# Optimization experiments

Hardware: AMD Instinct MI355X
Metric: run time of the kernel (lower is better)

## Reference

```python
import jax, jax.numpy as jnp
import numpy as np

N_NODES = 100000
N_EDGES = 1200000
IN_FEATS = 64
OUT_FEATS = 64


def setup_inputs() -> dict:
    key = jax.random.key(0)
    k1, k2, k3, k4 = jax.random.split(key, 4)
    feature = jax.random.normal(k1, (N_NODES, IN_FEATS), dtype=jnp.float32)
    edge_src = jax.random.randint(k2, (N_EDGES,), 0, N_NODES, dtype=jnp.int32)
    edge_dst = jax.random.randint(k3, (N_EDGES,), 0, N_NODES, dtype=jnp.int32)
    # xavier_normal_ init for linear weight (fan_in=fan_out=64)
    std = float(np.sqrt(2.0 / (IN_FEATS + OUT_FEATS)))
    W = jax.random.normal(k4, (OUT_FEATS, IN_FEATS), dtype=jnp.float32) * std
    b = jnp.zeros((OUT_FEATS,), dtype=jnp.float32)
    return {"feature": feature, "edge_src": edge_src, "edge_dst": edge_dst, "W": W, "b": b}


def reference(feature, edge_src, edge_dst, W, b):
    # copy_src: gather source-node features per edge, then mean-reduce by dst.
    msgs = feature[edge_src]                                   # [E, d_in]
    summed = jax.ops.segment_sum(msgs, edge_dst, num_segments=N_NODES)  # [N, d_in]
    deg = jax.ops.segment_sum(jnp.ones((edge_src.shape[0],), feature.dtype),
                              edge_dst, num_segments=N_NODES)  # [N]
    h = summed / jnp.maximum(deg, 1.0)[:, None]                # mean; 0 for isolated nodes
    # apply_nodes: linear + activation
    h = jnp.einsum("nd,od->no", h, W) + b
    return jax.nn.relu(h)
```

## Files before the change

### kernel.cpp

```cpp
#include <hip/hip_runtime.h>


typedef __attribute__((ext_vector_type(8))) short short8;
typedef __attribute__((ext_vector_type(4))) float floatx4;

constexpr int kNodes = 100000;
constexpr int kEdges = 1200000;

constexpr int kBucketShift = 7;
constexpr int kBucketNodes = 1 << kBucketShift;
constexpr int kBuckets = (kNodes + kBucketNodes - 1) >> kBucketShift;

constexpr int kBinBlocks = 128;
constexpr int kEdgesPerBlock = kEdges / kBinBlocks;
constexpr int kEPT = (kEdgesPerBlock + 1023) / 1024;

constexpr int kCap = 3072;
constexpr float kFxScale = 262144.0f;
constexpr int kAccStride = 68;

constexpr int kWsFeat   = 0;
constexpr int kWsOff    = 3200000;
constexpr int kWsBinned = kWsOff + kBinBlocks * 784;

__device__ __forceinline__ unsigned bf16rne(float f) {
  unsigned u = __float_as_uint(f);
  return (u + 0x7fffu + ((u >> 16) & 1u)) >> 16;
}

__global__ __launch_bounds__(1024) void gcn_build(
    const float* __restrict__ feat,
    const int* __restrict__ src, const int* __restrict__ dst,
    int* __restrict__ ws) {
  uint2* fb16  = (uint2*)(ws + kWsFeat);
  int* offT   = ws + kWsOff;
  int* binned = ws + kWsBinned;

  __shared__ int lhist[kBuckets];
  __shared__ int sm[1024];
  __shared__ int lcur[kBuckets];

  const int tid = threadIdx.x;
  for (int i = tid; i < kBuckets; i += 1024) lhist[i] = 0;
  __syncthreads();

  const int e0 = blockIdx.x * kEdgesPerBlock;
  int es[kEPT], ed[kEPT];
  #pragma unroll
  for (int k = 0; k < kEPT; ++k) {
    const int j = tid + k * 1024;
    if (j < kEdgesPerBlock) {
      es[k] = src[e0 + j];
      ed[k] = dst[e0 + j];
      atomicAdd(&lhist[ed[k] >> kBucketShift], 1);
    }
  }

  const int t = blockIdx.x * 1024 + tid;
  for (int i = t; i < kNodes * 16; i += kBinBlocks * 1024) {
    const float* fr = feat + (size_t)(i >> 4) * 64 + (i & 15);
    uint2 p;
    p.x = bf16rne(fr[0])  | (bf16rne(fr[16]) << 16);
    p.y = bf16rne(fr[32]) | (bf16rne(fr[48]) << 16);
    fb16[i] = p;
  }
  __syncthreads();

  const int own = (tid < kBuckets) ? lhist[tid] : 0;
  sm[tid] = own;
  __syncthreads();
  for (int off = 1; off < 1024; off <<= 1) {
    int v = (tid >= off) ? sm[tid - off] : 0;
    __syncthreads();
    sm[tid] += v;
    __syncthreads();
  }
  const int excl = sm[tid] - own;
  if (tid < kBuckets) {
    lcur[tid] = excl;
    offT[blockIdx.x * 784 + tid] = excl;
  }
  if (tid == kBuckets) offT[blockIdx.x * 784 + kBuckets] = kEdgesPerBlock;
  __syncthreads();

  int* myBin = binned + blockIdx.x * kEdgesPerBlock;
  #pragma unroll
  for (int k = 0; k < kEPT; ++k) {
    const int j = tid + k * 1024;
    if (j < kEdgesPerBlock) {
      const int d = ed[k];
      const int pos = atomicAdd(&lcur[d >> kBucketShift], 1);
      myBin[pos] = es[k] | ((d & (kBucketNodes - 1)) << 17);
    }
  }
}

__global__ __launch_bounds__(1024) void gcn_aggregate(
    const int*   __restrict__ ws_in,
    const float* __restrict__ W,
    const float* __restrict__ b,
    float*       __restrict__ out) {
  const uint2* fb16  = (const uint2*)(ws_in + kWsFeat);
  const int* offT   = ws_in + kWsOff;
  const int* binned = ws_in + kWsBinned;

  __shared__ __align__(16) char uShared[kBucketNodes * 72 * 2];
  __shared__ int    accum[kBucketNodes * kAccStride];
  __shared__ int    lofs[kBucketNodes + 1];
  __shared__ int    lcur[kBucketNodes];
  __shared__ int    runL[kBinBlocks + 1];
  __shared__ int    runG[kBinBlocks];
  __shared__ int    ssm[kBinBlocks];
  __shared__ ushort Wb16[64 * 64];
  __shared__ float  bsh[64];
  int*    lsrc  = (int*)uShared;
  ushort* hsAll = (ushort*)uShared;

  const int tid = threadIdx.x;
  const int bkt = blockIdx.x;

  if (tid < kBucketNodes) lcur[tid] = 0;
  for (int i = tid; i < 4096; i += 1024) Wb16[i] = (ushort)bf16rne(W[i]);
  if (tid < 64) bsh[tid] = b[tid];
  for (int i = tid; i < kBucketNodes * kAccStride; i += 1024) accum[i] = 0;

  int len = 0;
  if (tid < kBinBlocks) {
    const int o0 = offT[tid * 784 + bkt];
    const int o1 = offT[tid * 784 + bkt + 1];
    len = o1 - o0;
    runG[tid] = tid * kEdgesPerBlock + o0;
    ssm[tid] = len;
  }
  __syncthreads();
  for (int off = 1; off < kBinBlocks; off <<= 1) {
    int v = 0;
    if (tid < kBinBlocks && tid >= off) v = ssm[tid - off];
    __syncthreads();
    if (tid < kBinBlocks) ssm[tid] += v;
    __syncthreads();
  }
  if (tid < kBinBlocks) runL[tid] = ssm[tid] - len;
  if (tid == kBinBlocks - 1) runL[kBinBlocks] = ssm[kBinBlocks - 1];
  __syncthreads();

  int sz = runL[kBinBlocks];
  if (sz > kCap) sz = kCap;

  auto mapRead = [&](int j) -> unsigned {
    int lo = 0, hi = kBinBlocks;
    #pragma unroll
    for (int it = 0; it < 7; ++it) {
      const int mid = (lo + hi) >> 1;
      if (runL[mid] <= j) lo = mid; else hi = mid;
    }
    return (unsigned)binned[runG[lo] + (j - runL[lo])];
  };

  const int j0 = tid, j1 = tid + 1024, j2 = tid + 2048;
  const bool va = j0 < sz, vb = j1 < sz, vc = j2 < sz;
  unsigned ea = 0, eb = 0, ec = 0;
  if (va) { ea = mapRead(j0); atomicAdd(&lcur[ea >> 17], 1); }
  if (vb) { eb = mapRead(j1); atomicAdd(&lcur[eb >> 17], 1); }
  if (vc) { ec = mapRead(j2); atomicAdd(&lcur[ec >> 17], 1); }
  __syncthreads();

  if (tid < 64) {
    const int a  = lcur[tid * 2];
    const int b2 = lcur[tid * 2 + 1];
    int s = a + b2;
    #pragma unroll
    for (int off = 1; off < 64; off <<= 1) {
      const int v = __shfl_up(s, off, 64);
      if (tid >= off) s += v;
    }
    const int ex1 = s - b2;
    const int ex0 = ex1 - a;
    lofs[tid * 2]     = ex0;
    lofs[tid * 2 + 1] = ex1;
    lcur[tid * 2]     = ex0;
    lcur[tid * 2 + 1] = ex1;
    if (tid == 63) lofs[kBucketNodes] = s;
  }
  __syncthreads();

  if (va) { const int p = atomicAdd(&lcur[ea >> 17], 1); lsrc[p] = (int)ea; }
  if (vb) { const int p = atomicAdd(&lcur[eb >> 17], 1); lsrc[p] = (int)eb; }
  if (vc) { const int p = atomicAdd(&lcur[ec >> 17], 1); lsrc[p] = (int)ec; }
  __syncthreads();

  const int wave = tid >> 6;
  const int lane = tid & 63;
  const int g = lane >> 4;
  const int c = lane & 15;
  {
    const int E0 = lofs[wave * 8];
    const int E1 = lofs[wave * 8 + 8];
    const int lenw = E1 - E0;
    const int jb = E0 + ((lenw * g) >> 2);
    const int je = E0 + ((lenw * (g + 1)) >> 2);
    for (int j = jb; j < je; ++j) {
      const unsigned e = (unsigned)lsrc[j];
      const int s  = (int)(e & 0x1FFFF);
      const int dL = (int)(e >> 17);
      const uint2 v = fb16[(size_t)s * 16 + c];
      int* row = accum + dL * kAccStride + c;
      atomicAdd(row + 0,  (int)(__uint_as_float(v.x << 16)          * kFxScale));
      atomicAdd(row + 16, (int)(__uint_as_float(v.x & 0xffff0000u) * kFxScale));
      atomicAdd(row + 32, (int)(__uint_as_float(v.y << 16)          * kFxScale));
      atomicAdd(row + 48, (int)(__uint_as_float(v.y & 0xffff0000u) * kFxScale));
    }
  }
  __syncthreads();

  {
    const int nd = tid >> 3;
    const int ch = tid & 7;
    const int dg = lofs[nd + 1] - lofs[nd];
    const float inv = 1.0f / (kFxScale * (float)(dg > 1 ? dg : 1));
    const int* arow = accum + nd * kAccStride + ch * 8;
    unsigned h[8];
    #pragma unroll
    for (int q = 0; q < 8; ++q) h[q] = bf16rne((float)arow[q] * inv);
    uint4 pk;
    pk.x = h[0] | (h[1] << 16);
    pk.y = h[2] | (h[3] << 16);
    pk.z = h[4] | (h[5] << 16);
    pk.w = h[6] | (h[7] << 16);
    *(uint4*)(hsAll + nd * 72 + ch * 8) = pk;
  }
  __syncthreads();

  if (tid < 512) {
    const int w8   = tid >> 6;
    const int ln   = tid & 63;
    const int quad = ln >> 4;
    const int col  = ln & 15;
    const int n0 = bkt << kBucketShift;

    const short8 a0 = *reinterpret_cast<const short8*>(
        hsAll + (w8 * 16 + col) * 72 + 0 * 32 + quad * 8);
    const short8 a1 = *reinterpret_cast<const short8*>(
        hsAll + (w8 * 16 + col) * 72 + 1 * 32 + quad * 8);

    #pragma unroll
    for (int ob = 0; ob < 4; ++ob) {
      const short8 b0 = *reinterpret_cast<const short8*>(
          Wb16 + (ob * 16 + col) * 64 + 0 * 32 + quad * 8);
      const short8 b1 = *reinterpret_cast<const short8*>(
          Wb16 + (ob * 16 + col) * 64 + 1 * 32 + quad * 8);
      floatx4 acc = {0.f, 0.f, 0.f, 0.f};
      acc = __builtin_amdgcn_mfma_f32_16x16x32_bf16(a0, b0, acc, 0, 0, 0);
      acc = __builtin_amdgcn_mfma_f32_16x16x32_bf16(a1, b1, acc, 0, 0, 0);

      const int o = ob * 16 + col;
      const float bo = bsh[o];
      #pragma unroll
      for (int r = 0; r < 4; ++r) {
        const int node = n0 + w8 * 16 + quad * 4 + r;
        if (node < kNodes) {
          const float v = acc[r] + bo;
          out[(size_t)node * 64 + o] = v > 0.0f ? v : 0.0f;
        }
      }
    }
  }
}

extern "C" void kernel_launch(void* const* d_in, const int* in_sizes, int n_in,
                              void* d_out, int out_size, void* d_ws, size_t ws_size,
                              hipStream_t stream) {
  const float* feature  = (const float*)d_in[0];
  const int*   edge_src = (const int*)  d_in[1];
  const int*   edge_dst = (const int*)  d_in[2];
  const float* W        = (const float*)d_in[3];
  const float* b        = (const float*)d_in[4];

  float* out = (float*)d_out;
  int*   ws  = (int*)d_ws;

  gcn_build<<<kBinBlocks, 1024, 0, stream>>>(feature, edge_src, edge_dst, ws);
  gcn_aggregate<<<kBuckets, 1024, 0, stream>>>(ws, W, b, out);
}
```

Before: 138.2 us.

## Accumulate per-node sums in registers instead of LDS fixed-point atomics

Assigns each 16-lane group two consecutive destination nodes within the bucket and sums their gathered bf16 source features in float registers, writing the mean directly to the bf16 staging tile. This removes the shared accumulator array, its zero-initialization, the fixed-point conversion and all per-edge LDS atomics. The trade-off is load imbalance, because work is split by node rather than evenly by edge count, and high-degree nodes serialize within a group. LDS footprint also shrinks.

```diff
diff --git a/kernel.cpp b/kernel.cpp
--- a/kernel.cpp
+++ b/kernel.cpp
@@ -16,8 +16,6 @@
 constexpr int kEPT = (kEdgesPerBlock + 1023) / 1024;
 
 constexpr int kCap = 3072;
-constexpr float kFxScale = 262144.0f;
-constexpr int kAccStride = 68;
 
 constexpr int kWsFeat   = 0;
 constexpr int kWsOff    = 3200000;
@@ -105,7 +103,6 @@
   const int* binned = ws_in + kWsBinned;
 
   __shared__ __align__(16) char uShared[kBucketNodes * 72 * 2];
-  __shared__ int    accum[kBucketNodes * kAccStride];
   __shared__ int    lofs[kBucketNodes + 1];
   __shared__ int    lcur[kBucketNodes];
   __shared__ int    runL[kBinBlocks + 1];
@@ -122,7 +119,6 @@
   if (tid < kBucketNodes) lcur[tid] = 0;
   for (int i = tid; i < 4096; i += 1024) Wb16[i] = (ushort)bf16rne(W[i]);
   if (tid < 64) bsh[tid] = b[tid];
-  for (int i = tid; i < kBucketNodes * kAccStride; i += 1024) accum[i] = 0;
 
   int len = 0;
   if (tid < kBinBlocks) {
@@ -193,41 +189,46 @@
   const int lane = tid & 63;
   const int g = lane >> 4;
   const int c = lane & 15;
+  const int nd0 = wave * 8 + g * 2;
+
+  float a00 = 0.f, a01 = 0.f, a02 = 0.f, a03 = 0.f;
+  float a10 = 0.f, a11 = 0.f, a12 = 0.f, a13 = 0.f;
+  const int sA = lofs[nd0];
+  const int sB = lofs[nd0 + 1];
+  const int sC = lofs[nd0 + 2];
+  for (int j = sA; j < sB; ++j) {
+    const unsigned e = (unsigned)lsrc[j];
+    const uint2 v = fb16[(size_t)(e & 0x1FFFF) * 16 + c];
+    a00 += __uint_as_float(v.x << 16);
+    a01 += __uint_as_float(v.x & 0xffff0000u);
+    a02 += __uint_as_float(v.y << 16);
+    a03 += __uint_as_float(v.y & 0xffff0000u);
+  }
+  for (int j = sB; j < sC; ++j) {
+    const unsigned e = (unsigned)lsrc[j];
+    const uint2 v = fb16[(size_t)(e & 0x1FFFF) * 16 + c];
+    a10 += __uint_as_float(v.x << 16);
+    a11 += __uint_as_float(v.x & 0xffff0000u);
+    a12 += __uint_as_float(v.y << 16);
+    a13 += __uint_as_float(v.y & 0xffff0000u);
+  }
+  __syncthreads();
+
   {
-    const int E0 = lofs[wave * 8];
-    const int E1 = lofs[wave * 8 + 8];
-    const int lenw = E1 - E0;
-    const int jb = E0 + ((lenw * g) >> 2);
-    const int je = E0 + ((lenw * (g + 1)) >> 2);
-    for (int j = jb; j < je; ++j) {
-      const unsigned e = (unsigned)lsrc[j];
-      const int s  = (int)(e & 0x1FFFF);
-      const int dL = (int)(e >> 17);
-      const uint2 v = fb16[(size_t)s * 16 + c];
-      int* row = accum + dL * kAccStride + c;
-      atomicAdd(row + 0,  (int)(__uint_as_float(v.x << 16)          * kFxScale));
-      atomicAdd(row + 16, (int)(__uint_as_float(v.x & 0xffff0000u) * kFxScale));
-      atomicAdd(row + 32, (int)(__uint_as_float(v.y << 16)          * kFxScale));
-      atomicAdd(row + 48, (int)(__uint_as_float(v.y & 0xffff0000u) * kFxScale));
-    }
-  }
-  __syncthreads();
-
-  {
-    const int nd = tid >> 3;
-    const int ch = tid & 7;
-    const int dg = lofs[nd + 1] - lofs[nd];
-    const float inv = 1.0f / (kFxScale * (float)(dg > 1 ? dg : 1));
-    const int* arow = accum + nd * kAccStride + ch * 8;
-    unsigned h[8];
-    #pragma unroll
-    for (int q = 0; q < 8; ++q) h[q] = bf16rne((float)arow[q] * inv);
-    uint4 pk;
-    pk.x = h[0] | (h[1] << 16);
-    pk.y = h[2] | (h[3] << 16);
-    pk.z = h[4] | (h[5] << 16);
-    pk.w = h[6] | (h[7] << 16);
-    *(uint4*)(hsAll + nd * 72 + ch * 8) = pk;
+    const int dg0 = sB - sA;
+    const int dg1 = sC - sB;
+    const float inv0 = 1.0f / (float)(dg0 > 1 ? dg0 : 1);
+    const float inv1 = 1.0f / (float)(dg1 > 1 ? dg1 : 1);
+    ushort* row0 = hsAll + nd0 * 72;
+    ushort* row1 = row0 + 72;
+    row0[c]      = (ushort)bf16rne(a00 * inv0);
+    row0[16 + c] = (ushort)bf16rne(a01 * inv0);
+    row0[32 + c] = (ushort)bf16rne(a02 * inv0);
+    row0[48 + c] = (ushort)bf16rne(a03 * inv0);
+    row1[c]      = (ushort)bf16rne(a10 * inv1);
+    row1[16 + c] = (ushort)bf16rne(a11 * inv1);
+    row1[32 + c] = (ushort)bf16rne(a12 * inv1);
+    row1[48 + c] = (ushort)bf16rne(a13 * inv1);
   }
   __syncthreads();
 
@@ -238,20 +239,20 @@
     const int col  = ln & 15;
     const int n0 = bkt << kBucketShift;
 
-    const short8 a0 = *reinterpret_cast<const short8*>(
+    const short8 af0 = *reinterpret_cast<const short8*>(
         hsAll + (w8 * 16 + col) * 72 + 0 * 32 + quad * 8);
-    const short8 a1 = *reinterpret_cast<const short8*>(
+    const short8 af1 = *reinterpret_cast<const short8*>(
         hsAll + (w8 * 16 + col) * 72 + 1 * 32 + quad * 8);
 
     #pragma unroll
     for (int ob = 0; ob < 4; ++ob) {
-      const short8 b0 = *reinterpret_cast<const short8*>(
+      const short8 bf0 = *reinterpret_cast<const short8*>(
           Wb16 + (ob * 16 + col) * 64 + 0 * 32 + quad * 8);
-      const short8 b1 = *reinterpret_cast<const short8*>(
+      const short8 bf1 = *reinterpret_cast<const short8*>(
           Wb16 + (ob * 16 + col) * 64 + 1 * 32 + quad * 8);
       floatx4 acc = {0.f, 0.f, 0.f, 0.f};
-      acc = __builtin_amdgcn_mfma_f32_16x16x32_bf16(a0, b0, acc, 0, 0, 0);
-      acc = __builtin_amdgcn_mfma_f32_16x16x32_bf16(a1, b1, acc, 0, 0, 0);
+      acc = __builtin_amdgcn_mfma_f32_16x16x32_bf16(af0, bf0, acc, 0, 0, 0);
+      acc = __builtin_amdgcn_mfma_f32_16x16x32_bf16(af1, bf1, acc, 0, 0, 0);
 
       const int o = ob * 16 + col;
       const float bo = bsh[o];
```

Measured after the change: 142.2 us. +2.9%, slower.

## Rebucket nodes into 1024 buckets of 98 and split edges evenly across slots

Applied to the files above, without the earlier changes.

Node buckets change from 128 power-of-two nodes (782 buckets) to 98 nodes (1024 buckets), so bucket count matches the 1024-thread block and the grid fills the GPU more evenly. The aggregate kernel drops the third edge slot (capacity 2048) and assigns edges uniformly to 64 slots instead of per-8-node wave ranges, which balances work but lets different slots hit the same destination rows. The bucket index now uses integer division by 98, and the GEMM tail pads to 112 rows with zeroed padding rows. Buckets with more than 2048 edges would silently drop edges.

```diff
diff --git a/kernel.cpp b/kernel.cpp
--- a/kernel.cpp
+++ b/kernel.cpp
@@ -7,21 +7,20 @@
 constexpr int kNodes = 100000;
 constexpr int kEdges = 1200000;
 
-constexpr int kBucketShift = 7;
-constexpr int kBucketNodes = 1 << kBucketShift;
-constexpr int kBuckets = (kNodes + kBucketNodes - 1) >> kBucketShift;
+constexpr int kBuckets = 1024;
+constexpr int kBucketNodes = 98;
 
 constexpr int kBinBlocks = 128;
 constexpr int kEdgesPerBlock = kEdges / kBinBlocks;
 constexpr int kEPT = (kEdgesPerBlock + 1023) / 1024;
 
-constexpr int kCap = 3072;
+constexpr int kCap = 2048;
 constexpr float kFxScale = 262144.0f;
 constexpr int kAccStride = 68;
 
 constexpr int kWsFeat   = 0;
 constexpr int kWsOff    = 3200000;
-constexpr int kWsBinned = kWsOff + kBinBlocks * 784;
+constexpr int kWsBinned = kWsOff + kBinBlocks * (kBuckets + 1);
 
 __device__ __forceinline__ unsigned bf16rne(float f) {
   unsigned u = __float_as_uint(f);
@@ -41,18 +40,21 @@
   __shared__ int lcur[kBuckets];
 
   const int tid = threadIdx.x;
-  for (int i = tid; i < kBuckets; i += 1024) lhist[i] = 0;
+  lhist[tid] = 0;
   __syncthreads();
 
   const int e0 = blockIdx.x * kEdgesPerBlock;
-  int es[kEPT], ed[kEPT];
+  int es[kEPT], ebk[kEPT], edl[kEPT];
   #pragma unroll
   for (int k = 0; k < kEPT; ++k) {
     const int j = tid + k * 1024;
     if (j < kEdgesPerBlock) {
       es[k] = src[e0 + j];
-      ed[k] = dst[e0 + j];
-      atomicAdd(&lhist[ed[k] >> kBucketShift], 1);
+      const int d = dst[e0 + j];
+      const int bk = d / kBucketNodes;
+      ebk[k] = bk;
+      edl[k] = d - bk * kBucketNodes;
+      atomicAdd(&lhist[bk], 1);
     }
   }
 
@@ -66,7 +68,7 @@
   }
   __syncthreads();
 
-  const int own = (tid < kBuckets) ? lhist[tid] : 0;
+  const int own = lhist[tid];
   sm[tid] = own;
   __syncthreads();
   for (int off = 1; off < 1024; off <<= 1) {
@@ -76,11 +78,9 @@
     __syncthreads();
   }
   const int excl = sm[tid] - own;
-  if (tid < kBuckets) {
-    lcur[tid] = excl;
-    offT[blockIdx.x * 784 + tid] = excl;
-  }
-  if (tid == kBuckets) offT[blockIdx.x * 784 + kBuckets] = kEdgesPerBlock;
+  lcur[tid] = excl;
+  offT[blockIdx.x * (kBuckets + 1) + tid] = excl;
+  if (tid == 0) offT[blockIdx.x * (kBuckets + 1) + kBuckets] = kEdgesPerBlock;
   __syncthreads();
 
   int* myBin = binned + blockIdx.x * kEdgesPerBlock;
@@ -88,9 +88,8 @@
   for (int k = 0; k < kEPT; ++k) {
     const int j = tid + k * 1024;
     if (j < kEdgesPerBlock) {
-      const int d = ed[k];
-      const int pos = atomicAdd(&lcur[d >> kBucketShift], 1);
-      myBin[pos] = es[k] | ((d & (kBucketNodes - 1)) << 17);
+      const int pos = atomicAdd(&lcur[ebk[k]], 1);
+      myBin[pos] = es[k] | (edl[k] << 17);
     }
   }
 }
@@ -104,10 +103,10 @@
   const int* offT   = ws_in + kWsOff;
   const int* binned = ws_in + kWsBinned;
 
-  __shared__ __align__(16) char uShared[kBucketNodes * 72 * 2];
+  __shared__ __align__(16) char uShared[112 * 72 * 2];
   __shared__ int    accum[kBucketNodes * kAccStride];
-  __shared__ int    lofs[kBucketNodes + 1];
-  __shared__ int    lcur[kBucketNodes];
+  __shared__ int    lofs[129];
+  __shared__ int    lcur[128];
   __shared__ int    runL[kBinBlocks + 1];
   __shared__ int    runG[kBinBlocks];
   __shared__ int    ssm[kBinBlocks];
@@ -119,15 +118,15 @@
   const int tid = threadIdx.x;
   const int bkt = blockIdx.x;
 
-  if (tid < kBucketNodes) lcur[tid] = 0;
+  if (tid < 128) lcur[tid] = 0;
   for (int i = tid; i < 4096; i += 1024) Wb16[i] = (ushort)bf16rne(W[i]);
   if (tid < 64) bsh[tid] = b[tid];
   for (int i = tid; i < kBucketNodes * kAccStride; i += 1024) accum[i] = 0;
 
   int len = 0;
   if (tid < kBinBlocks) {
-    const int o0 = offT[tid * 784 + bkt];
-    const int o1 = offT[tid * 784 + bkt + 1];
+    const int o0 = offT[tid * (kBuckets + 1) + bkt];
+    const int o1 = offT[tid * (kBuckets + 1) + bkt + 1];
     len = o1 - o0;
     runG[tid] = tid * kEdgesPerBlock + o0;
     ssm[tid] = len;
@@ -157,12 +156,11 @@
     return (unsigned)binned[runG[lo] + (j - runL[lo])];
   };
 
-  const int j0 = tid, j1 = tid + 1024, j2 = tid + 2048;
-  const bool va = j0 < sz, vb = j1 < sz, vc = j2 < sz;
-  unsigned ea = 0, eb = 0, ec = 0;
+  const int j0 = tid, j1 = tid + 1024;
+  const bool va = j0 < sz, vb = j1 < sz;
+  unsigned ea = 0, eb = 0;
   if (va) { ea = mapRead(j0); atomicAdd(&lcur[ea >> 17], 1); }
   if (vb) { eb = mapRead(j1); atomicAdd(&lcur[eb >> 17], 1); }
-  if (vc) { ec = mapRead(j2); atomicAdd(&lcur[ec >> 17], 1); }
   __syncthreads();
 
   if (tid < 64) {
@@ -180,13 +178,12 @@
     lofs[tid * 2 + 1] = ex1;
     lcur[tid * 2]     = ex0;
     lcur[tid * 2 + 1] = ex1;
-    if (tid == 63) lofs[kBucketNodes] = s;
+    if (tid == 63) lofs[128] = s;
   }
   __syncthreads();
 
   if (va) { const int p = atomicAdd(&lcur[ea >> 17], 1); lsrc[p] = (int)ea; }
   if (vb) { const int p = atomicAdd(&lcur[eb >> 17], 1); lsrc[p] = (int)eb; }
-  if (vc) { const int p = atomicAdd(&lcur[ec >> 17], 1); lsrc[p] = (int)ec; }
   __syncthreads();
 
   const int wave = tid >> 6;
@@ -194,11 +191,9 @@
   const int g = lane >> 4;
   const int c = lane & 15;
   {
-    const int E0 = lofs[wave * 8];
-    const int E1 = lofs[wave * 8 + 8];
-    const int lenw = E1 - E0;
-    const int jb = E0 + ((lenw * g) >> 2);
-    const int je = E0 + ((lenw * (g + 1)) >> 2);
+    const int slot = wave * 4 + g;
+    const int jb = (sz * slot) >> 6;
+    const int je = (sz * (slot + 1)) >> 6;
     for (int j = jb; j < je; ++j) {
       const unsigned e = (unsigned)lsrc[j];
       const int s  = (int)(e & 0x1FFFF);
@@ -216,49 +211,55 @@
   {
     const int nd = tid >> 3;
     const int ch = tid & 7;
-    const int dg = lofs[nd + 1] - lofs[nd];
-    const float inv = 1.0f / (kFxScale * (float)(dg > 1 ? dg : 1));
-    const int* arow = accum + nd * kAccStride + ch * 8;
-    unsigned h[8];
-    #pragma unroll
-    for (int q = 0; q < 8; ++q) h[q] = bf16rne((float)arow[q] * inv);
-    uint4 pk;
-    pk.x = h[0] | (h[1] << 16);
-    pk.y = h[2] | (h[3] << 16);
-    pk.z = h[4] | (h[5] << 16);
-    pk.w = h[6] | (h[7] << 16);
-    *(uint4*)(hsAll + nd * 72 + ch * 8) = pk;
-  }
-  __syncthreads();
-
-  if (tid < 512) {
+    if (nd < kBucketNodes) {
+      const int dg = lofs[nd + 1] - lofs[nd];
+      const float inv = 1.0f / (kFxScale * (float)(dg > 1 ? dg : 1));
+      const int* arow = accum + nd * kAccStride + ch * 8;
+      unsigned h[8];
+      #pragma unroll
+      for (int q = 0; q < 8; ++q) h[q] = bf16rne((float)arow[q] * inv);
+      uint4 pk;
+      pk.x = h[0] | (h[1] << 16);
+      pk.y = h[2] | (h[3] << 16);
+      pk.z = h[4] | (h[5] << 16);
+      pk.w = h[6] | (h[7] << 16);
+      *(uint4*)(hsAll + nd * 72 + ch * 8) = pk;
+    } else {
+      if (nd < 112) *(uint4*)(hsAll + nd * 72 + ch * 8) =
+          make_uint4(0u, 0u, 0u, 0u);
+    }
+  }
+  __syncthreads();
+
+  if (tid < 448) {
     const int w8   = tid >> 6;
     const int ln   = tid & 63;
     const int quad = ln >> 4;
     const int col  = ln & 15;
-    const int n0 = bkt << kBucketShift;
-
-    const short8 a0 = *reinterpret_cast<const short8*>(
+    const int n0 = bkt * kBucketNodes;
+
+    const short8 af0 = *reinterpret_cast<const short8*>(
         hsAll + (w8 * 16 + col) * 72 + 0 * 32 + quad * 8);
-    const short8 a1 = *reinterpret_cast<const short8*>(
+    const short8 af1 = *reinterpret_cast<const short8*>(
         hsAll + (w8 * 16 + col) * 72 + 1 * 32 + quad * 8);
 
     #pragma unroll
     for (int ob = 0; ob < 4; ++ob) {
-      const short8 b0 = *reinterpret_cast<const short8*>(
+      const short8 bf0 = *reinterpret_cast<const short8*>(
           Wb16 + (ob * 16 + col) * 64 + 0 * 32 + quad * 8);
-      const short8 b1 = *reinterpret_cast<const short8*>(
+      const short8 bf1 = *reinterpret_cast<const short8*>(
           Wb16 + (ob * 16 + col) * 64 + 1 * 32 + quad * 8);
       floatx4 acc = {0.f, 0.f, 0.f, 0.f};
-      acc = __builtin_amdgcn_mfma_f32_16x16x32_bf16(a0, b0, acc, 0, 0, 0);
-      acc = __builtin_amdgcn_mfma_f32_16x16x32_bf16(a1, b1, acc, 0, 0, 0);
+      acc = __builtin_amdgcn_mfma_f32_16x16x32_bf16(af0, bf0, acc, 0, 0, 0);
+      acc = __builtin_amdgcn_mfma_f32_16x16x32_bf16(af1, bf1, acc, 0, 0, 0);
 
       const int o = ob * 16 + col;
       const float bo = bsh[o];
       #pragma unroll
       for (int r = 0; r < 4; ++r) {
-        const int node = n0 + w8 * 16 + quad * 4 + r;
-        if (node < kNodes) {
+        const int local = w8 * 16 + quad * 4 + r;
+        const int node = n0 + local;
+        if (local < kBucketNodes && node < kNodes) {
           const float v = acc[r] + bo;
           out[(size_t)node * 64 + o] = v > 0.0f ? v : 0.0f;
         }
```

Result: no change. 137.6 us (median of 2 runs) (-0.4%).
